# Kernel optimization log

Hardware: AMD Instinct MI355X
Metric: run time of the kernel (lower is better)

## Reference

```python
import jax, jax.numpy as jnp
import numpy as np

B, S, T = 256, 512, 20
VOCAB, E, H, SKIP = 100000, 25, 128, 64


def _lstm_scan(x, skip, mask, K, R, Sk, b):
    # x:[S,B,E], skip:[S,B,SKIP], mask:[S,B] bool. Keras RNN mask semantics:
    # masked steps carry previous h/c and emit previous h.
    Bn = x.shape[1]
    Hn = R.shape[0]
    def step(carry, inp):
        h, c = carry
        xt, st, mt = inp
        z = xt @ K + h @ R + st @ Sk + b            # [B,4H]
        zi, zf, zg, zo = jnp.split(z, 4, axis=-1)
        cn = jax.nn.sigmoid(zf) * c + jax.nn.sigmoid(zi) * jnp.tanh(zg)
        hn = jax.nn.sigmoid(zo) * jnp.tanh(cn)
        m = mt[:, None]
        h2 = jnp.where(m, hn, h)
        c2 = jnp.where(m, cn, c)
        return (h2, c2), h2
    init = (jnp.zeros((Bn, Hn), x.dtype), jnp.zeros((Bn, Hn), x.dtype))
    (hF, cF), hs = jax.lax.scan(step, init, (x, skip, mask))
    return hs, hF


def setup_inputs() -> dict:
    key = jax.random.key(0)
    ks = jax.random.split(key, 20)
    p = lambda k, shp: jax.random.normal(k, shp, dtype=jnp.float32) * 0.05
    inp = {
        "input_tags": jax.random.randint(ks[0], (B, S, T), 0, VOCAB, dtype=jnp.int32),
        "embedded_skips": jax.random.normal(ks[1], (B, S, SKIP), dtype=jnp.float32),
        "emb_table": p(ks[2], (VOCAB, E)),
        "kernel_f": p(ks[3], (E, 4 * H)),
        "rec_f": p(ks[4], (H, 4 * H)),
        "skip_f": p(ks[5], (SKIP, 4 * H)),
        "bias_f": jnp.zeros((4 * H,), jnp.float32),
        "kernel_b": p(ks[6], (E, 4 * H)),
        "rec_b": p(ks[7], (H, 4 * H)),
        "skip_b": p(ks[8], (SKIP, 4 * H)),
        "bias_b": jnp.zeros((4 * H,), jnp.float32),
        "Wk": p(ks[9], (2 * H, H)),
        "bk": jnp.zeros((H,), jnp.float32),
        "Wq": p(ks[10], (H, H)),
        "bq": jnp.zeros((H,), jnp.float32),
        "We": p(ks[11], (H, 1)),
        "be": jnp.zeros((1,), jnp.float32),
    }
    return inp


def reference(input_tags, embedded_skips, emb_table,
              kernel_f, rec_f, skip_f, bias_f,
              kernel_b, rec_b, skip_b, bias_b,
              Wk, bk, Wq, bq, We, be):
    mask3 = input_tags != 0                          # [B,S,T]
    emb = emb_table[input_tags]                      # [B,S,T,E]
    num_mask = mask3.astype(emb.dtype)
    summed = jnp.sum(emb * num_mask[..., None], axis=2)   # [B,S,E]
    denom = jnp.sum(num_mask, axis=2)                     # [B,S]
    denom = jnp.where(denom == 0, jnp.ones_like(denom), denom)
    gru_inp = summed / denom[..., None]                   # [B,S,E]
    step_mask = mask3[:, :, 0]                            # [B,S]

    # time-major for scan
    x_t = jnp.swapaxes(gru_inp, 0, 1)
    s_t = jnp.swapaxes(embedded_skips, 0, 1)
    m_t = jnp.swapaxes(step_mask, 0, 1)

    hs_f, h_fwd = _lstm_scan(x_t, s_t, m_t, kernel_f, rec_f, skip_f, bias_f)
    hs_b_rev, _ = _lstm_scan(x_t[::-1], s_t[::-1], m_t[::-1], kernel_b, rec_b, skip_b, bias_b)
    hs_b = hs_b_rev[::-1]
    out = jnp.swapaxes(jnp.concatenate([hs_f, hs_b], axis=-1), 0, 1)  # [B,S,2H]

    keys = out @ Wk + bk                                  # [B,S,H]
    queries = (h_fwd @ Wq + bq)[:, None, :]               # [B,1,H]
    energy = jnp.tanh(keys + queries) @ We + be           # [B,S,1]
    energy = energy + (1.0 - step_mask.astype(energy.dtype))[..., None] * -1e9
    weights = jax.nn.softmax(energy, axis=1)
    context = jnp.sum(weights * out, axis=1)              # [B,2H]
    return context
```

## Files before the change

### kernel.cpp

```cpp
#include <hip/hip_runtime.h>
#include <math.h>

#define Bb 256
#define Ss 512
#define Tt 20
#define Ee 25
#define Hh 128
#define SKIPn 64
#define H4n 512
#define BSn (Bb*Ss)
#define MG 4
#define HP 160
#define LOG2E 1.4426950408889634f

typedef _Float16 f16x8 __attribute__((ext_vector_type(8)));
typedef float f32x4 __attribute__((ext_vector_type(4)));

__device__ __forceinline__ float rcpf(float x) { return __builtin_amdgcn_rcpf(x); }
__device__ __forceinline__ float exp2f_(float x) { return __builtin_amdgcn_exp2f(x); }

__device__ __forceinline__ void lgkm_barrier() {
    __asm__ __volatile__("" ::: "memory");
    __builtin_amdgcn_s_waitcnt(0xC07F);
    __builtin_amdgcn_s_barrier();
    __asm__ __volatile__("" ::: "memory");
}

__global__ void pool_kernel(const int* __restrict__ tags,
                            const float* __restrict__ table,
                            _Float16* __restrict__ gru16, float* __restrict__ maskf,
                            float* __restrict__ maskt) {
    int group = blockIdx.x * 8 + (threadIdx.x >> 5);
    int lane = threadIdx.x & 31;
    if (group >= BSn) return;
    int b = group >> 9;
    int t = group & (Ss - 1);
    const int* tg = tags + (size_t)group * Tt;
    const int el = (lane < Ee) ? lane : (Ee - 1);

    int tagv[Tt];
#pragma unroll
    for (int tt = 0; tt < Tt; tt++) tagv[tt] = tg[tt];

    float vv[Tt];
#pragma unroll
    for (int tt = 0; tt < Tt; tt++)
        vv[tt] = table[(size_t)tagv[tt] * Ee + el];

    float acc = 0.0f;
    int cnt = 0;
#pragma unroll
    for (int tt = 0; tt < Tt; tt++) {
        const bool nz = (tagv[tt] != 0);
        cnt += nz ? 1 : 0;
        acc += nz ? vv[tt] : 0.0f;
    }
    float scale = rcpf((float)(cnt > 0 ? cnt : 1));
    float v = (lane < Ee) ? acc * scale : 0.0f;
    gru16[((size_t)t * Bb + b) * 32 + lane] = (_Float16)v;
    if (lane == 0) {
        float m = (tagv[0] != 0) ? 1.0f : 0.0f;
        maskf[group] = m;
        maskt[(size_t)t * Bb + b] = m;
    }
}

__global__ void __launch_bounds__(256)
cvt_kernel(const float* __restrict__ in, _Float16* __restrict__ out) {
    size_t i = ((size_t)blockIdx.x * 256 + threadIdx.x) * 8;
    f32x4 a = *(const f32x4*)(in + i);
    f32x4 b = *(const f32x4*)(in + i + 4);
    f16x8 o;
#pragma unroll
    for (int j = 0; j < 4; j++) { o[j] = (_Float16)a[j]; o[j + 4] = (_Float16)b[j]; }
    *(f16x8*)(out + i) = o;
}

__global__ void __launch_bounds__(512)
__attribute__((amdgpu_waves_per_eu(2, 2)))
scan_kernel(const _Float16* __restrict__ gru16, const _Float16* __restrict__ skips16,
            const float* __restrict__ maskt,
            const float* __restrict__ Kf, const float* __restrict__ Rf,
            const float* __restrict__ Skf, const float* __restrict__ bf,
            const float* __restrict__ Kb, const float* __restrict__ Rb,
            const float* __restrict__ Skb, const float* __restrict__ bb,
            _Float16* __restrict__ hs16, float* __restrict__ hfwd)
{
    __shared__ __align__(16) _Float16 h16[2 * MG * HP];

    const int tid = threadIdx.x;
    const int lane = tid & 63;
    const int w = tid >> 6;
    const int l16 = lane & 15;
    const int q = lane >> 4;
    const int mb = l16 >> 2;
    const int bg = blockIdx.x & 63;
    const int dir = blockIdx.x >> 6;
    const int b0 = bg * MG;
    const int col = 16 * w + l16;

    const float* Kw = dir ? Kb : Kf;
    const float* Rw = dir ? Rb : Rf;
    const float* Sw = dir ? Skb : Skf;
    const float* bw = dir ? bb : bf;

    const float gs[4] = {LOG2E, LOG2E, 2.0f * LOG2E, LOG2E};

    f16x8 bfr[7][4];
#pragma unroll
    for (int kt = 0; kt < 7; kt++) {
#pragma unroll
        for (int g = 0; g < 4; g++) {
            const int n = g * Hh + col;
            f16x8 v;
#pragma unroll
            for (int j = 0; j < 8; j++) {
                const int k = 32 * kt + 8 * q + j;
                float x;
                if (k < 32)        x = (k < Ee) ? Kw[k * H4n + n] : 0.0f;
                else if (k < 160)  x = Rw[(k - 32) * H4n + n];
                else               x = Sw[(k - 160) * H4n + n];
                v[j] = (_Float16)(x * gs[g]);
            }
            bfr[kt][g] = v;
        }
    }
    float biasv[4];
#pragma unroll
    for (int g = 0; g < 4; g++) biasv[g] = bw[g * Hh + col] * gs[g];

    for (int idx = tid; idx < 2 * MG * HP; idx += 512) h16[idx] = (_Float16)0.0f;

    const _Float16* srow = skips16 + (size_t)(b0 + mb) * Ss * SKIPn;
    float c = 0.0f, h = 0.0f;

    _Float16* hsp = hs16 + ((size_t)(b0 + q) * Ss + (dir ? Ss - 1 : 0)) * (2 * Hh)
                    + dir * Hh + col;
    const ptrdiff_t odelta = dir ? -(2 * Hh) : (2 * Hh);

    auto issue_xs = [&](f16x8& xf, f16x8& s0, f16x8& s1, int i) {
        const int ii = (i < Ss) ? i : (Ss - 1);
        const int t = dir ? (Ss - 1 - ii) : ii;
        xf = *(const f16x8*)(gru16 + ((size_t)t * Bb + b0 + mb) * 32 + 8 * q);
        const _Float16* sp = srow + (size_t)t * SKIPn;
        s0 = *(const f16x8*)(sp + 8 * q);
        s1 = *(const f16x8*)(sp + 32 + 8 * q);
    };
    auto issue_m = [&](float& mk, int i) {
        const int ii = (i < Ss) ? i : (Ss - 1);
        const int t = dir ? (Ss - 1 - ii) : ii;
        mk = maskt[(size_t)t * Bb + b0 + q];
    };

    f16x8 xA, xB, sA0, sA1, sB0, sB1;
    float mA, mB;
    issue_xs(xA, sA0, sA1, 0); issue_m(mA, 0);
    issue_xs(xB, sB0, sB1, 1); issue_m(mB, 1);
    __syncthreads();

    auto body = [&](int i, f16x8& xf, f16x8& s0, f16x8& s1, float& mkv) {
        const _Float16* hb = h16 + (i & 1) * (MG * HP);
        const f16x8 ah0 = *(const f16x8*)(hb + mb * HP +  0 + 8 * q);
        const f16x8 ah1 = *(const f16x8*)(hb + mb * HP + 32 + 8 * q);
        const f16x8 ah2 = *(const f16x8*)(hb + mb * HP + 64 + 8 * q);
        const f16x8 ah3 = *(const f16x8*)(hb + mb * HP + 96 + 8 * q);

        f32x4 acc[4];
#pragma unroll
        for (int g = 0; g < 4; g++) {
            f32x4 a = {biasv[g], biasv[g], biasv[g], biasv[g]};
            acc[g] = a;
        }
#pragma unroll
        for (int g = 0; g < 4; g++) {
            acc[g] = __builtin_amdgcn_mfma_f32_16x16x32_f16(xf, bfr[0][g], acc[g], 0, 0, 0);
            acc[g] = __builtin_amdgcn_mfma_f32_16x16x32_f16(s0, bfr[5][g], acc[g], 0, 0, 0);
            acc[g] = __builtin_amdgcn_mfma_f32_16x16x32_f16(s1, bfr[6][g], acc[g], 0, 0, 0);
        }
        issue_xs(xf, s0, s1, i + 2);
#pragma unroll
        for (int g = 0; g < 4; g++) {
            acc[g] = __builtin_amdgcn_mfma_f32_16x16x32_f16(ah0, bfr[1][g], acc[g], 0, 0, 0);
            acc[g] = __builtin_amdgcn_mfma_f32_16x16x32_f16(ah1, bfr[2][g], acc[g], 0, 0, 0);
            acc[g] = __builtin_amdgcn_mfma_f32_16x16x32_f16(ah2, bfr[3][g], acc[g], 0, 0, 0);
            acc[g] = __builtin_amdgcn_mfma_f32_16x16x32_f16(ah3, bfr[4][g], acc[g], 0, 0, 0);
        }

        const float mk = mkv;
        issue_m(mkv, i + 2);
        const float zi = acc[0][0], zf = acc[1][0], zg = acc[2][0], zo = acc[3][0];
        const float ei = exp2f_(fminf(-zi, 88.0f));
        const float ef = exp2f_(fminf(-zf, 88.0f));
        const float eg = exp2f_(fminf(-zg, 88.0f));
        const float eo = exp2f_(fminf(-zo, 88.0f));
        const float pi = 1.0f + ei, pg = 1.0f + eg, pf = 1.0f + ef;
        const float p  = pi * pg;
        const float t1 = (1.0f - eg) * pf;
        const float cn = fmaf(c, p, t1) * rcpf(pf * p);
        const float ec = exp2f_(fminf(cn * (-2.0f * LOG2E), 88.0f));
        const float hn = (1.0f - ec) * rcpf((1.0f + eo) * (1.0f + ec));
        const bool mm = (mk != 0.0f);
        c = mm ? cn : c;
        h = mm ? hn : h;

        _Float16* hw = h16 + ((i + 1) & 1) * (MG * HP);
        hw[q * HP + col] = (_Float16)h;
        *hsp = (_Float16)h;
        hsp += odelta;
        lgkm_barrier();
    };

#pragma unroll 1
    for (int i = 0; i < Ss; i += 2) {
        body(i,     xA, sA0, sA1, mA);
        body(i + 1, xB, sB0, sB1, mB);
    }

    if (dir == 0) hfwd[(size_t)(b0 + q) * Hh + col] = h;
}

__global__ void __launch_bounds__(512)
attn_kernel(const _Float16* __restrict__ hs16, const float* __restrict__ hfwd,
            const float* __restrict__ Wq, const float* __restrict__ bq,
            const float* __restrict__ bk,
            const float* __restrict__ Wk, const float* __restrict__ We,
            const float* __restrict__ maskf, float* __restrict__ outp)
{
    __shared__ float hfl[Hh];
    __shared__ float qpart[4][Hh];
    __shared__ float qtot_s[Hh];
    __shared__ float epart[8][Ss];
    __shared__ float ws2[Ss];
    __shared__ float redm[8], reds[8];
    __shared__ float ctxp[16][2 * Hh + 1];

    const int tid = threadIdx.x;
    const int lane = tid & 63;
    const int w = tid >> 6;
    const int l16 = lane & 15;
    const int q = lane >> 4;
    const int b = blockIdx.x;
    const int j = 16 * w + l16;

    f16x8 bk16[8];
#pragma unroll
    for (int kt = 0; kt < 8; kt++) {
        f16x8 v;
#pragma unroll
        for (int jj = 0; jj < 8; jj++)
            v[jj] = (_Float16)Wk[(32 * kt + 8 * q + jj) * Hh + j];
        bk16[kt] = v;
    }
    const float wej = We[j];

    if (tid < Hh) hfl[tid] = hfwd[(size_t)b * Hh + tid];
    __syncthreads();
    {
        const int jj = tid & 127, seg = tid >> 7;
        float p = 0.0f;
#pragma unroll
        for (int k = 0; k < 32; k++)
            p += hfl[32 * seg + k] * Wq[(32 * seg + k) * Hh + jj];
        qpart[seg][jj] = p;
    }
    __syncthreads();
    if (tid < Hh)
        qtot_s[tid] = qpart[0][tid] + qpart[1][tid] + qpart[2][tid] + qpart[3][tid]
                      + bq[tid] + bk[tid];
    __syncthreads();
    const float qj = qtot_s[j];

    const _Float16* hb = hs16 + (size_t)b * Ss * (2 * Hh);
#pragma unroll 1
    for (int st = 0; st < 32; st++) {
        const int s0 = st * 16;
        const _Float16* arow = hb + (size_t)(s0 + l16) * (2 * Hh) + 8 * q;
        f32x4 acc = {0.f, 0.f, 0.f, 0.f};
#pragma unroll
        for (int kt = 0; kt < 8; kt++) {
            const f16x8 a = *(const f16x8*)(arow + 32 * kt);
            acc = __builtin_amdgcn_mfma_f32_16x16x32_f16(a, bk16[kt], acc, 0, 0, 0);
        }
        float vals[4];
#pragma unroll
        for (int r = 0; r < 4; r++) {
            const float x = acc[r] + qj;
            const float e = exp2f_(fminf(x * (-2.0f * LOG2E), 80.0f));
            vals[r] = (1.0f - e) * rcpf(1.0f + e) * wej;
        }
#pragma unroll
        for (int m = 1; m < 16; m <<= 1) {
#pragma unroll
            for (int r = 0; r < 4; r++) vals[r] += __shfl_xor(vals[r], m);
        }
        if (l16 == 0) {
#pragma unroll
            for (int r = 0; r < 4; r++) epart[w][s0 + 4 * q + r] = vals[r];
        }
    }
    __syncthreads();

    {
        float e = 0.0f;
#pragma unroll
        for (int ww = 0; ww < 8; ww++) e += epart[ww][tid];
        e += (1.0f - maskf[(size_t)b * Ss + tid]) * -1e9f;
        float mx = e;
#pragma unroll
        for (int off = 32; off > 0; off >>= 1) mx = fmaxf(mx, __shfl_xor(mx, off));
        if (lane == 0) redm[w] = mx;
        __syncthreads();
        mx = redm[0];
#pragma unroll
        for (int ww = 1; ww < 8; ww++) mx = fmaxf(mx, redm[ww]);
        const float p = exp2f_((e - mx) * LOG2E);
        float sm = p;
#pragma unroll
        for (int off = 32; off > 0; off >>= 1) sm += __shfl_xor(sm, off);
        if (lane == 0) reds[w] = sm;
        __syncthreads();
        sm = reds[0] + reds[1] + reds[2] + reds[3] + reds[4] + reds[5] + reds[6] + reds[7];
        ws2[(tid & 31) * 16 + (tid >> 5)] = p * rcpf(sm);
    }
    __syncthreads();

    {
        const int cg = tid >> 4;
        const int seg = tid & 15;
        float a[8];
#pragma unroll
        for (int jj = 0; jj < 8; jj++) a[jj] = 0.0f;
#pragma unroll 4
        for (int sg = 0; sg < 32; sg++) {
            const int s = seg * 32 + sg;
            const float wv = ws2[sg * 16 + seg];
            const f16x8 hv = *(const f16x8*)(hb + (size_t)s * (2 * Hh) + 8 * cg);
#pragma unroll
            for (int jj = 0; jj < 8; jj++) a[jj] = fmaf(wv, (float)hv[jj], a[jj]);
        }
#pragma unroll
        for (int jj = 0; jj < 8; jj++) ctxp[seg][8 * cg + jj] = a[jj];
    }
    __syncthreads();
    if (tid < 2 * Hh) {
        float s = 0.0f;
#pragma unroll
        for (int seg = 0; seg < 16; seg++) s += ctxp[seg][tid];
        outp[(size_t)b * (2 * Hh) + tid] = s;
    }
}

extern "C" void kernel_launch(void* const* d_in, const int* in_sizes, int n_in,
                              void* d_out, int out_size, void* d_ws, size_t ws_size,
                              hipStream_t stream) {
    const int*   tags  = (const int*)d_in[0];
    const float* skips = (const float*)d_in[1];
    const float* table = (const float*)d_in[2];
    const float* Kf    = (const float*)d_in[3];
    const float* Rf    = (const float*)d_in[4];
    const float* Skf   = (const float*)d_in[5];
    const float* bf    = (const float*)d_in[6];
    const float* Kb    = (const float*)d_in[7];
    const float* Rb    = (const float*)d_in[8];
    const float* Skb   = (const float*)d_in[9];
    const float* bb    = (const float*)d_in[10];
    const float* Wk    = (const float*)d_in[11];
    const float* bk    = (const float*)d_in[12];
    const float* Wq    = (const float*)d_in[13];
    const float* bq    = (const float*)d_in[14];
    const float* We    = (const float*)d_in[15];

    char* ws = (char*)d_ws;
    _Float16* gru16   = (_Float16*)ws; ws += (size_t)BSn * 32 * 2;
    _Float16* skips16 = (_Float16*)ws; ws += (size_t)BSn * SKIPn * 2;
    float* maskf  = (float*)ws;  ws += (size_t)BSn * 4;
    float* maskt  = (float*)ws;  ws += (size_t)BSn * 4;
    _Float16* hs16 = (_Float16*)ws; ws += (size_t)BSn * 2 * Hh * 2;
    float* hfwd   = (float*)ws;  ws += (size_t)Bb * Hh * 4;

    pool_kernel<<<BSn / 8, 256, 0, stream>>>(tags, table, gru16, maskf, maskt);
    cvt_kernel<<<BSn * SKIPn / (256 * 8), 256, 0, stream>>>(skips, skips16);
    scan_kernel<<<128, 512, 0, stream>>>(gru16, skips16, maskt,
                                         Kf, Rf, Skf, bf,
                                         Kb, Rb, Skb, bb,
                                         hs16, hfwd);
    attn_kernel<<<Bb, 512, 0, stream>>>(hs16, hfwd, Wq, bq, bk, Wk, We, maskf,
                                        (float*)d_out);
}
```

Baseline: 551.3 us.

## Precompute input/skip gate projections in a parallel GEMM before the LSTM scan

Splits the LSTM into a fully parallel MFMA kernel that computes x@K + skip@Sk + bias for all timesteps into an fp16 z buffer. A lighter scan kernel then only does the recurrent h@R matmul per step and loads the precomputed gates with a prefetch two steps ahead. This takes the input and skip projections off the serial critical path of the 512-step recurrence. The cost is a large fp16 intermediate buffer, extra memory traffic and fp16 rounding of the gate preactivations. There are fallbacks for a chunked variant with carry state and for the original fused scan, chosen by workspace size.

```diff
diff --git a/kernel.cpp b/kernel.cpp
--- a/kernel.cpp
+++ b/kernel.cpp
@@ -11,9 +11,11 @@
 #define BSn (Bb*Ss)
 #define MG 4
 #define HP 160
+#define ZROWS 256
 #define LOG2E 1.4426950408889634f
 
 typedef _Float16 f16x8 __attribute__((ext_vector_type(8)));
+typedef _Float16 f16x4 __attribute__((ext_vector_type(4)));
 typedef float f32x4 __attribute__((ext_vector_type(4)));
 
 __device__ __forceinline__ float rcpf(float x) { return __builtin_amdgcn_rcpf(x); }
@@ -65,26 +67,249 @@
     }
 }
 
+template<bool TR>
 __global__ void __launch_bounds__(256)
 cvt_kernel(const float* __restrict__ in, _Float16* __restrict__ out) {
-    size_t i = ((size_t)blockIdx.x * 256 + threadIdx.x) * 8;
-    f32x4 a = *(const f32x4*)(in + i);
-    f32x4 b = *(const f32x4*)(in + i + 4);
-    f16x8 o;
-#pragma unroll
-    for (int j = 0; j < 4; j++) { o[j] = (_Float16)a[j]; o[j + 4] = (_Float16)b[j]; }
-    *(f16x8*)(out + i) = o;
-}
-
+    size_t id = (size_t)blockIdx.x * 256 + threadIdx.x;
+    if (TR) {
+        size_t bt = id >> 3;
+        const int c8 = (int)(id & 7);
+        const int b = (int)(bt >> 9);
+        const int t = (int)(bt & (Ss - 1));
+        const float* ip = in + bt * SKIPn + c8 * 8;
+        f32x4 a = *(const f32x4*)(ip);
+        f32x4 bv = *(const f32x4*)(ip + 4);
+        f16x8 o;
+#pragma unroll
+        for (int j = 0; j < 4; j++) { o[j] = (_Float16)a[j]; o[j + 4] = (_Float16)bv[j]; }
+        *(f16x8*)(out + ((size_t)t * Bb + b) * SKIPn + c8 * 8) = o;
+    } else {
+        size_t i = id * 8;
+        f32x4 a = *(const f32x4*)(in + i);
+        f32x4 bv = *(const f32x4*)(in + i + 4);
+        f16x8 o;
+#pragma unroll
+        for (int j = 0; j < 4; j++) { o[j] = (_Float16)a[j]; o[j + 4] = (_Float16)bv[j]; }
+        *(f16x8*)(out + i) = o;
+    }
+}
+
+template<int CH>
+__global__ void __launch_bounds__(512)
+zxs_kernel(const _Float16* __restrict__ gru16, const _Float16* __restrict__ sk16,
+           const float* __restrict__ Kf, const float* __restrict__ Skf, const float* __restrict__ bf,
+           const float* __restrict__ Kb, const float* __restrict__ Skb, const float* __restrict__ bb,
+           _Float16* __restrict__ zbuf, int k)
+{
+    const int tid = threadIdx.x;
+    const int lane = tid & 63;
+    const int w = tid >> 6;
+    const int l16 = lane & 15;
+    const int q = lane >> 4;
+    const int dir = blockIdx.x & 1;
+    const int rg = blockIdx.x >> 1;
+    const size_t lrow0 = (size_t)rg * ZROWS;
+    const size_t grow0 = ((size_t)(dir ? (Ss - CH * (k + 1)) : (CH * k)) * Bb) + lrow0;
+    const int col = 16 * w + l16;
+
+    const float* Kw = dir ? Kb : Kf;
+    const float* Sw = dir ? Skb : Skf;
+    const float* bw = dir ? bb : bf;
+    const float gs[4] = {LOG2E, LOG2E, 2.0f * LOG2E, LOG2E};
+
+    f16x8 bx[4], bs0[4], bs1[4];
+#pragma unroll
+    for (int g = 0; g < 4; g++) {
+        const int n = g * Hh + col;
+        f16x8 vx, v0, v1;
+#pragma unroll
+        for (int j = 0; j < 8; j++) {
+            const int kk = 8 * q + j;
+            vx[j] = (_Float16)(((kk < Ee) ? Kw[kk * H4n + n] : 0.0f) * gs[g]);
+            v0[j] = (_Float16)(Sw[kk * H4n + n] * gs[g]);
+            v1[j] = (_Float16)(Sw[(32 + kk) * H4n + n] * gs[g]);
+        }
+        bx[g] = vx; bs0[g] = v0; bs1[g] = v1;
+    }
+    float biasv[4];
+#pragma unroll
+    for (int g = 0; g < 4; g++) biasv[g] = bw[g * Hh + col] * gs[g];
+
+    auto lda = [&](f16x8& ax, f16x8& a0, f16x8& a1, int ch) {
+        const size_t r = grow0 + 16 * ch + l16;
+        ax = *(const f16x8*)(gru16 + r * 32 + 8 * q);
+        a0 = *(const f16x8*)(sk16 + r * SKIPn + 8 * q);
+        a1 = *(const f16x8*)(sk16 + r * SKIPn + 32 + 8 * q);
+    };
+
+    f16x8 ax, a0, a1, nx, n0, n1;
+    lda(ax, a0, a1, 0);
+#pragma unroll 1
+    for (int ch = 0; ch < ZROWS / 16; ch++) {
+        const int chn = (ch + 1 < ZROWS / 16) ? ch + 1 : ch;
+        lda(nx, n0, n1, chn);
+        f32x4 acc[4];
+#pragma unroll
+        for (int g = 0; g < 4; g++) {
+            f32x4 a = {biasv[g], biasv[g], biasv[g], biasv[g]};
+            acc[g] = a;
+        }
+#pragma unroll
+        for (int g = 0; g < 4; g++)
+            acc[g] = __builtin_amdgcn_mfma_f32_16x16x32_f16(ax, bx[g], acc[g], 0, 0, 0);
+#pragma unroll
+        for (int g = 0; g < 4; g++)
+            acc[g] = __builtin_amdgcn_mfma_f32_16x16x32_f16(a0, bs0[g], acc[g], 0, 0, 0);
+#pragma unroll
+        for (int g = 0; g < 4; g++)
+            acc[g] = __builtin_amdgcn_mfma_f32_16x16x32_f16(a1, bs1[g], acc[g], 0, 0, 0);
+
+        _Float16* op = zbuf + (((size_t)dir * CH * Bb + lrow0 + 16 * ch + 4 * q) * 128 + col) * 4;
+#pragma unroll
+        for (int r = 0; r < 4; r++) {
+            f16x4 o;
+#pragma unroll
+            for (int g = 0; g < 4; g++) o[g] = (_Float16)acc[g][r];
+            *(f16x4*)(op + (size_t)r * 512) = o;
+        }
+        ax = nx; a0 = n0; a1 = n1;
+    }
+}
+
+template<int CH>
 __global__ void __launch_bounds__(512)
 __attribute__((amdgpu_waves_per_eu(2, 2)))
-scan_kernel(const _Float16* __restrict__ gru16, const _Float16* __restrict__ skips16,
-            const float* __restrict__ maskt,
-            const float* __restrict__ Kf, const float* __restrict__ Rf,
-            const float* __restrict__ Skf, const float* __restrict__ bf,
-            const float* __restrict__ Kb, const float* __restrict__ Rb,
-            const float* __restrict__ Skb, const float* __restrict__ bb,
-            _Float16* __restrict__ hs16, float* __restrict__ hfwd)
+scan_split(const _Float16* __restrict__ zbuf, const float* __restrict__ maskt,
+           const float* __restrict__ Rf, const float* __restrict__ Rb,
+           _Float16* __restrict__ hs16, float* __restrict__ hfwd,
+           float2* __restrict__ carry, int k)
+{
+    constexpr int NCH = Ss / CH;
+    __shared__ __align__(16) _Float16 h16[2 * MG * HP];
+
+    const int tid = threadIdx.x;
+    const int lane = tid & 63;
+    const int w = tid >> 6;
+    const int l16 = lane & 15;
+    const int q = lane >> 4;
+    const int mb = l16 >> 2;
+    const int bg = blockIdx.x & 63;
+    const int dir = blockIdx.x >> 6;
+    const int b0 = bg * MG;
+    const int col = 16 * w + l16;
+
+    const float* Rw = dir ? Rb : Rf;
+    const float gs[4] = {LOG2E, LOG2E, 2.0f * LOG2E, LOG2E};
+
+    f16x8 hfr[4][4];
+#pragma unroll
+    for (int kt = 0; kt < 4; kt++) {
+#pragma unroll
+        for (int g = 0; g < 4; g++) {
+            const int n = g * Hh + col;
+            f16x8 v;
+#pragma unroll
+            for (int j = 0; j < 8; j++)
+                v[j] = (_Float16)(Rw[(32 * kt + 8 * q + j) * H4n + n] * gs[g]);
+            hfr[kt][g] = v;
+        }
+    }
+
+    const int cid = (dir * Bb + b0 + q) * Hh + col;
+    float c = 0.0f, h = 0.0f;
+    if (k > 0) { float2 hc = carry[cid]; h = hc.x; c = hc.y; }
+
+    h16[q * HP + col] = (_Float16)h;
+
+    const _Float16* zbase = zbuf + ((size_t)dir * CH * Bb + (size_t)(b0 + q)) * 512 + col * 4;
+
+    const int t0 = dir ? (Ss - 1 - CH * k) : (CH * k);
+    _Float16* hsp = hs16 + ((size_t)(b0 + q) * Ss + t0) * (2 * Hh) + dir * Hh + col;
+    const ptrdiff_t odelta = dir ? -(2 * Hh) : (2 * Hh);
+
+    auto issue_z = [&](f16x4& z, int i) {
+        const int ii = (i < CH) ? i : (CH - 1);
+        const int tl = dir ? (CH - 1 - ii) : ii;
+        z = *(const f16x4*)(zbase + (size_t)tl * (Bb * 512));
+    };
+    auto issue_m = [&](float& mk, int i) {
+        const int ii = (i < CH) ? i : (CH - 1);
+        const int tg = dir ? (Ss - 1 - CH * k - ii) : (CH * k + ii);
+        mk = maskt[(size_t)tg * Bb + b0 + q];
+    };
+
+    f16x4 zA, zB;
+    float mA, mB;
+    issue_z(zA, 0); issue_m(mA, 0);
+    issue_z(zB, 1); issue_m(mB, 1);
+    __syncthreads();
+
+    auto body = [&](int i, f16x4& zf4, float& mkv) {
+        const _Float16* hb = h16 + (i & 1) * (MG * HP);
+        const f16x8 ah0 = *(const f16x8*)(hb + mb * HP +  0 + 8 * q);
+        const f16x8 ah1 = *(const f16x8*)(hb + mb * HP + 32 + 8 * q);
+        const f16x8 ah2 = *(const f16x8*)(hb + mb * HP + 64 + 8 * q);
+        const f16x8 ah3 = *(const f16x8*)(hb + mb * HP + 96 + 8 * q);
+
+        f32x4 acc[4];
+#pragma unroll
+        for (int g = 0; g < 4; g++) {
+            const float zv = (float)zf4[g];
+            f32x4 a = {zv, zv, zv, zv};
+            acc[g] = a;
+        }
+        issue_z(zf4, i + 2);
+#pragma unroll
+        for (int g = 0; g < 4; g++) {
+            acc[g] = __builtin_amdgcn_mfma_f32_16x16x32_f16(ah0, hfr[0][g], acc[g], 0, 0, 0);
+            acc[g] = __builtin_amdgcn_mfma_f32_16x16x32_f16(ah1, hfr[1][g], acc[g], 0, 0, 0);
+            acc[g] = __builtin_amdgcn_mfma_f32_16x16x32_f16(ah2, hfr[2][g], acc[g], 0, 0, 0);
+            acc[g] = __builtin_amdgcn_mfma_f32_16x16x32_f16(ah3, hfr[3][g], acc[g], 0, 0, 0);
+        }
+
+        const float mk = mkv;
+        issue_m(mkv, i + 2);
+        const float zi = acc[0][0], zf = acc[1][0], zg = acc[2][0], zo = acc[3][0];
+        const float ei = exp2f_(fminf(-zi, 88.0f));
+        const float ef = exp2f_(fminf(-zf, 88.0f));
+        const float eg = exp2f_(fminf(-zg, 88.0f));
+        const float eo = exp2f_(fminf(-zo, 88.0f));
+        const float pi = 1.0f + ei, pg = 1.0f + eg, pf = 1.0f + ef;
+        const float p  = pi * pg;
+        const float t1 = (1.0f - eg) * pf;
+        const float cn = fmaf(c, p, t1) * rcpf(pf * p);
+        const float ec = exp2f_(fminf(cn * (-2.0f * LOG2E), 88.0f));
+        const float hn = (1.0f - ec) * rcpf((1.0f + eo) * (1.0f + ec));
+        const bool mm = (mk != 0.0f);
+        c = mm ? cn : c;
+        h = mm ? hn : h;
+
+        _Float16* hw = h16 + ((i + 1) & 1) * (MG * HP);
+        hw[q * HP + col] = (_Float16)h;
+        *hsp = (_Float16)h;
+        hsp += odelta;
+        lgkm_barrier();
+    };
+
+#pragma unroll 1
+    for (int i = 0; i < CH; i += 2) {
+        body(i,     zA, mA);
+        body(i + 1, zB, mB);
+    }
+
+    if (k + 1 < NCH) carry[cid] = make_float2(h, c);
+    if (dir == 0 && k + 1 == NCH) hfwd[(size_t)(b0 + q) * Hh + col] = h;
+}
+
+__global__ void __launch_bounds__(512)
+__attribute__((amdgpu_waves_per_eu(2, 2)))
+scan_fused(const _Float16* __restrict__ gru16, const _Float16* __restrict__ skips16,
+           const float* __restrict__ maskt,
+           const float* __restrict__ Kf, const float* __restrict__ Rf,
+           const float* __restrict__ Skf, const float* __restrict__ bf,
+           const float* __restrict__ Kb, const float* __restrict__ Rb,
+           const float* __restrict__ Skb, const float* __restrict__ bb,
+           _Float16* __restrict__ hs16, float* __restrict__ hfwd)
 {
     __shared__ __align__(16) _Float16 h16[2 * MG * HP];
 
@@ -370,20 +595,73 @@
     const float* bq    = (const float*)d_in[14];
     const float* We    = (const float*)d_in[15];
 
+    const size_t SZ_GRU = (size_t)BSn * 32 * 2;
+    const size_t SZ_SKT = (size_t)BSn * SKIPn * 2;
+    const size_t SZ_HS  = (size_t)BSn * 2 * Hh * 2;
+    const size_t SZ_MSK = (size_t)BSn * 4;
+    const size_t SZ_HF  = (size_t)Bb * Hh * 4;
+    const size_t SZ_CAR = (size_t)2 * Bb * Hh * 8;
+    const size_t SZ_ZF  = (size_t)2 * Ss * Bb * 512 * 2;
+    const size_t SZ_ZC  = (size_t)2 * 128 * Bb * 512 * 2;
+
+    const size_t NEED_FULL  = SZ_ZF + SZ_HS + 2 * SZ_MSK + SZ_HF;
+    const size_t NEED_CHUNK = SZ_ZC + SZ_GRU + SZ_SKT + SZ_HS + 2 * SZ_MSK + SZ_HF + SZ_CAR;
+
     char* ws = (char*)d_ws;
-    _Float16* gru16   = (_Float16*)ws; ws += (size_t)BSn * 32 * 2;
-    _Float16* skips16 = (_Float16*)ws; ws += (size_t)BSn * SKIPn * 2;
-    float* maskf  = (float*)ws;  ws += (size_t)BSn * 4;
-    float* maskt  = (float*)ws;  ws += (size_t)BSn * 4;
-    _Float16* hs16 = (_Float16*)ws; ws += (size_t)BSn * 2 * Hh * 2;
-    float* hfwd   = (float*)ws;  ws += (size_t)Bb * Hh * 4;
-
-    pool_kernel<<<BSn / 8, 256, 0, stream>>>(tags, table, gru16, maskf, maskt);
-    cvt_kernel<<<BSn * SKIPn / (256 * 8), 256, 0, stream>>>(skips, skips16);
-    scan_kernel<<<128, 512, 0, stream>>>(gru16, skips16, maskt,
-                                         Kf, Rf, Skf, bf,
-                                         Kb, Rb, Skb, bb,
-                                         hs16, hfwd);
-    attn_kernel<<<Bb, 512, 0, stream>>>(hs16, hfwd, Wq, bq, bk, Wk, We, maskf,
-                                        (float*)d_out);
-}
+
+    if (ws_size >= NEED_FULL) {
+        _Float16* zbuf  = (_Float16*)ws; ws += SZ_ZF;
+        _Float16* hs16  = (_Float16*)ws;
+        _Float16* gru16 = (_Float16*)ws;
+        _Float16* sk16t = (_Float16*)(ws + SZ_GRU);
+        ws += SZ_HS;
+        float* maskf = (float*)ws; ws += SZ_MSK;
+        float* maskt = (float*)ws; ws += SZ_MSK;
+        float* hfwd  = (float*)ws; ws += SZ_HF;
+
+        pool_kernel<<<BSn / 8, 256, 0, stream>>>(tags, table, gru16, maskf, maskt);
+        cvt_kernel<true><<<BSn * SKIPn / (256 * 8), 256, 0, stream>>>(skips, sk16t);
+        zxs_kernel<Ss><<<2 * (Ss * Bb / ZROWS), 512, 0, stream>>>(
+            gru16, sk16t, Kf, Skf, bf, Kb, Skb, bb, zbuf, 0);
+        scan_split<Ss><<<128, 512, 0, stream>>>(zbuf, maskt, Rf, Rb, hs16, hfwd,
+                                                (float2*)hfwd , 0);
+        attn_kernel<<<Bb, 512, 0, stream>>>(hs16, hfwd, Wq, bq, bk, Wk, We, maskf,
+                                            (float*)d_out);
+    } else if (ws_size >= NEED_CHUNK) {
+        _Float16* zbuf  = (_Float16*)ws; ws += SZ_ZC;
+        _Float16* gru16 = (_Float16*)ws; ws += SZ_GRU;
+        _Float16* sk16t = (_Float16*)ws; ws += SZ_SKT;
+        _Float16* hs16  = (_Float16*)ws; ws += SZ_HS;
+        float* maskf = (float*)ws; ws += SZ_MSK;
+        float* maskt = (float*)ws; ws += SZ_MSK;
+        float* hfwd  = (float*)ws; ws += SZ_HF;
+        float2* carry = (float2*)ws; ws += SZ_CAR;
+
+        pool_kernel<<<BSn / 8, 256, 0, stream>>>(tags, table, gru16, maskf, maskt);
+        cvt_kernel<true><<<BSn * SKIPn / (256 * 8), 256, 0, stream>>>(skips, sk16t);
+        for (int k = 0; k < 4; k++) {
+            zxs_kernel<128><<<2 * (128 * Bb / ZROWS), 512, 0, stream>>>(
+                gru16, sk16t, Kf, Skf, bf, Kb, Skb, bb, zbuf, k);
+            scan_split<128><<<128, 512, 0, stream>>>(zbuf, maskt, Rf, Rb, hs16, hfwd,
+                                                     carry, k);
+        }
+        attn_kernel<<<Bb, 512, 0, stream>>>(hs16, hfwd, Wq, bq, bk, Wk, We, maskf,
+                                            (float*)d_out);
+    } else {
+        _Float16* gru16   = (_Float16*)ws; ws += SZ_GRU;
+        _Float16* skips16 = (_Float16*)ws; ws += SZ_SKT;
+        float* maskf = (float*)ws; ws += SZ_MSK;
+        float* maskt = (float*)ws; ws += SZ_MSK;
+        _Float16* hs16 = (_Float16*)ws; ws += SZ_HS;
+        float* hfwd  = (float*)ws; ws += SZ_HF;
+
+        pool_kernel<<<BSn / 8, 256, 0, stream>>>(tags, table, gru16, maskf, maskt);
+        cvt_kernel<false><<<BSn * SKIPn / (256 * 8), 256, 0, stream>>>(skips, skips16);
+        scan_fused<<<128, 512, 0, stream>>>(gru16, skips16, maskt,
+                                            Kf, Rf, Skf, bf,
+                                            Kb, Rb, Skb, bb,
+                                            hs16, hfwd);
+        attn_kernel<<<Bb, 512, 0, stream>>>(hs16, hfwd, Wq, bq, bk, Wk, We, maskf,
+                                            (float*)d_out);
+    }
+}
```

After: 599.9 us. 8.8% more time.

## Precompute input projections per 16-step chunk in LDS; stage attention tiles through LDS

Applied to the files above, without the earlier changes.

The scan kernel stops doing the x and skip input-projection MFMAs inside every serial step. Instead it computes them in batches of 16 timesteps into an LDS buffer in fp16, so each recurrent step only runs the four hidden-state MFMAs per gate plus one LDS read. This shortens the serial critical path and lowers register pressure, at the cost of fp16 rounding of the pre-activations and an extra barrier per chunk. The attention kernel double-buffers its hs tiles through LDS with a prefetch of the next tile, and the context-reduction thread mapping is changed. The mask buffer gets padding so that prefetches past the end stay in bounds.

```diff
diff --git a/kernel.cpp b/kernel.cpp
--- a/kernel.cpp
+++ b/kernel.cpp
@@ -11,9 +11,12 @@
 #define BSn (Bb*Ss)
 #define MG 4
 #define HP 160
+#define ZP 520
+#define AP 264
 #define LOG2E 1.4426950408889634f
 
 typedef _Float16 f16x8 __attribute__((ext_vector_type(8)));
+typedef _Float16 f16x4 __attribute__((ext_vector_type(4)));
 typedef float f32x4 __attribute__((ext_vector_type(4)));
 
 __device__ __forceinline__ float rcpf(float x) { return __builtin_amdgcn_rcpf(x); }
@@ -78,7 +81,7 @@
 
 __global__ void __launch_bounds__(512)
 __attribute__((amdgpu_waves_per_eu(2, 2)))
-scan_kernel(const _Float16* __restrict__ gru16, const _Float16* __restrict__ skips16,
+scan_kernel(const _Float16* __restrict__ gru16, const _Float16* __restrict__ sk16,
             const float* __restrict__ maskt,
             const float* __restrict__ Kf, const float* __restrict__ Rf,
             const float* __restrict__ Skf, const float* __restrict__ bf,
@@ -87,6 +90,7 @@
             _Float16* __restrict__ hs16, float* __restrict__ hfwd)
 {
     __shared__ __align__(16) _Float16 h16[2 * MG * HP];
+    __shared__ __align__(16) _Float16 zlds[64 * ZP];
 
     const int tid = threadIdx.x;
     const int lane = tid & 63;
@@ -103,92 +107,90 @@
     const float* Rw = dir ? Rb : Rf;
     const float* Sw = dir ? Skb : Skf;
     const float* bw = dir ? bb : bf;
-
     const float gs[4] = {LOG2E, LOG2E, 2.0f * LOG2E, LOG2E};
 
-    f16x8 bfr[7][4];
-#pragma unroll
-    for (int kt = 0; kt < 7; kt++) {
+    f16x8 hfr[4][4];
+#pragma unroll
+    for (int kt = 0; kt < 4; kt++) {
 #pragma unroll
         for (int g = 0; g < 4; g++) {
             const int n = g * Hh + col;
             f16x8 v;
 #pragma unroll
-            for (int j = 0; j < 8; j++) {
-                const int k = 32 * kt + 8 * q + j;
-                float x;
-                if (k < 32)        x = (k < Ee) ? Kw[k * H4n + n] : 0.0f;
-                else if (k < 160)  x = Rw[(k - 32) * H4n + n];
-                else               x = Sw[(k - 160) * H4n + n];
-                v[j] = (_Float16)(x * gs[g]);
-            }
-            bfr[kt][g] = v;
-        }
-    }
-    float biasv[4];
-#pragma unroll
-    for (int g = 0; g < 4; g++) biasv[g] = bw[g * Hh + col] * gs[g];
+            for (int j = 0; j < 8; j++)
+                v[j] = (_Float16)(Rw[(32 * kt + 8 * q + j) * H4n + n] * gs[g]);
+            hfr[kt][g] = v;
+        }
+    }
+    f16x8 bx[4], bs0[4], bs1[4];
+    f32x4 biasA[4];
+#pragma unroll
+    for (int g = 0; g < 4; g++) {
+        const int n = g * Hh + col;
+        f16x8 vx, v0, v1;
+#pragma unroll
+        for (int j = 0; j < 8; j++) {
+            const int kk = 8 * q + j;
+            vx[j] = (_Float16)(((kk < Ee) ? Kw[kk * H4n + n] : 0.0f) * gs[g]);
+            v0[j] = (_Float16)(Sw[kk * H4n + n] * gs[g]);
+            v1[j] = (_Float16)(Sw[(32 + kk) * H4n + n] * gs[g]);
+        }
+        bx[g] = vx; bs0[g] = v0; bs1[g] = v1;
+        const float bv = bw[g * Hh + col] * gs[g];
+        f32x4 ba = {bv, bv, bv, bv};
+        biasA[g] = ba;
+    }
+    const f32x4 zacc4 = {0.0f, 0.0f, 0.0f, 0.0f};
 
     for (int idx = tid; idx < 2 * MG * HP; idx += 512) h16[idx] = (_Float16)0.0f;
 
-    const _Float16* srow = skips16 + (size_t)(b0 + mb) * Ss * SKIPn;
     float c = 0.0f, h = 0.0f;
+
+    const int tsub = l16 >> 2, bbn = l16 & 3;
+    const int tg0 = dir ? (Ss - 1 - tsub) : tsub;
+    const _Float16* px = gru16 + ((size_t)tg0 * Bb + b0 + bbn) * 32 + 8 * q;
+    const _Float16* ps = sk16 + ((size_t)(b0 + bbn) * Ss + tg0) * SKIPn + 8 * q;
+    const ptrdiff_t pxd = (dir ? -4 : 4) * (ptrdiff_t)(Bb * 32);
+    const ptrdiff_t psd = (dir ? -4 : 4) * (ptrdiff_t)SKIPn;
+
+    const float* mptr = maskt + (size_t)(dir ? (Ss - 1) : 0) * Bb + b0 + q;
+    const ptrdiff_t mdelta = dir ? -(ptrdiff_t)Bb : (ptrdiff_t)Bb;
+    float mA = mptr[0], mB = mptr[mdelta];
+    const float* mpf = mptr + 2 * mdelta;
 
     _Float16* hsp = hs16 + ((size_t)(b0 + q) * Ss + (dir ? Ss - 1 : 0)) * (2 * Hh)
                     + dir * Hh + col;
     const ptrdiff_t odelta = dir ? -(2 * Hh) : (2 * Hh);
 
-    auto issue_xs = [&](f16x8& xf, f16x8& s0, f16x8& s1, int i) {
-        const int ii = (i < Ss) ? i : (Ss - 1);
-        const int t = dir ? (Ss - 1 - ii) : ii;
-        xf = *(const f16x8*)(gru16 + ((size_t)t * Bb + b0 + mb) * 32 + 8 * q);
-        const _Float16* sp = srow + (size_t)t * SKIPn;
-        s0 = *(const f16x8*)(sp + 8 * q);
-        s1 = *(const f16x8*)(sp + 32 + 8 * q);
-    };
-    auto issue_m = [&](float& mk, int i) {
-        const int ii = (i < Ss) ? i : (Ss - 1);
-        const int t = dir ? (Ss - 1 - ii) : ii;
-        mk = maskt[(size_t)t * Bb + b0 + q];
-    };
-
-    f16x8 xA, xB, sA0, sA1, sB0, sB1;
-    float mA, mB;
-    issue_xs(xA, sA0, sA1, 0); issue_m(mA, 0);
-    issue_xs(xB, sB0, sB1, 1); issue_m(mB, 1);
-    __syncthreads();
-
-    auto body = [&](int i, f16x8& xf, f16x8& s0, f16x8& s1, float& mkv) {
+    f16x8 nax = *(const f16x8*)px;
+    f16x8 na0 = *(const f16x8*)ps;
+    f16x8 na1 = *(const f16x8*)(ps + 32);
+
+    __syncthreads();
+
+    auto body = [&](int i, float& mkv) {
         const _Float16* hb = h16 + (i & 1) * (MG * HP);
         const f16x8 ah0 = *(const f16x8*)(hb + mb * HP +  0 + 8 * q);
         const f16x8 ah1 = *(const f16x8*)(hb + mb * HP + 32 + 8 * q);
         const f16x8 ah2 = *(const f16x8*)(hb + mb * HP + 64 + 8 * q);
         const f16x8 ah3 = *(const f16x8*)(hb + mb * HP + 96 + 8 * q);
+        const f16x4 z4 = *(const f16x4*)(zlds + ((i & 15) * 4 + q) * ZP + col * 4);
 
         f32x4 acc[4];
 #pragma unroll
         for (int g = 0; g < 4; g++) {
-            f32x4 a = {biasv[g], biasv[g], biasv[g], biasv[g]};
-            acc[g] = a;
-        }
-#pragma unroll
-        for (int g = 0; g < 4; g++) {
-            acc[g] = __builtin_amdgcn_mfma_f32_16x16x32_f16(xf, bfr[0][g], acc[g], 0, 0, 0);
-            acc[g] = __builtin_amdgcn_mfma_f32_16x16x32_f16(s0, bfr[5][g], acc[g], 0, 0, 0);
-            acc[g] = __builtin_amdgcn_mfma_f32_16x16x32_f16(s1, bfr[6][g], acc[g], 0, 0, 0);
-        }
-        issue_xs(xf, s0, s1, i + 2);
-#pragma unroll
-        for (int g = 0; g < 4; g++) {
-            acc[g] = __builtin_amdgcn_mfma_f32_16x16x32_f16(ah0, bfr[1][g], acc[g], 0, 0, 0);
-            acc[g] = __builtin_amdgcn_mfma_f32_16x16x32_f16(ah1, bfr[2][g], acc[g], 0, 0, 0);
-            acc[g] = __builtin_amdgcn_mfma_f32_16x16x32_f16(ah2, bfr[3][g], acc[g], 0, 0, 0);
-            acc[g] = __builtin_amdgcn_mfma_f32_16x16x32_f16(ah3, bfr[4][g], acc[g], 0, 0, 0);
+            acc[g] = __builtin_amdgcn_mfma_f32_16x16x32_f16(ah0, hfr[0][g], zacc4, 0, 0, 0);
+            acc[g] = __builtin_amdgcn_mfma_f32_16x16x32_f16(ah1, hfr[1][g], acc[g], 0, 0, 0);
+            acc[g] = __builtin_amdgcn_mfma_f32_16x16x32_f16(ah2, hfr[2][g], acc[g], 0, 0, 0);
+            acc[g] = __builtin_amdgcn_mfma_f32_16x16x32_f16(ah3, hfr[3][g], acc[g], 0, 0, 0);
         }
 
         const float mk = mkv;
-        issue_m(mkv, i + 2);
-        const float zi = acc[0][0], zf = acc[1][0], zg = acc[2][0], zo = acc[3][0];
+        mkv = *mpf; mpf += mdelta;
+        const float zi = acc[0][0] + (float)z4[0];
+        const float zf = acc[1][0] + (float)z4[1];
+        const float zg = acc[2][0] + (float)z4[2];
+        const float zo = acc[3][0] + (float)z4[3];
         const float ei = exp2f_(fminf(-zi, 88.0f));
         const float ef = exp2f_(fminf(-zf, 88.0f));
         const float eg = exp2f_(fminf(-zg, 88.0f));
@@ -210,10 +212,41 @@
         lgkm_barrier();
     };
 
+    int i = 0;
 #pragma unroll 1
-    for (int i = 0; i < Ss; i += 2) {
-        body(i,     xA, sA0, sA1, mA);
-        body(i + 1, xB, sB0, sB1, mB);
+    for (int k = 0; k < 32; ++k) {
+#pragma unroll
+        for (int tile = 0; tile < 4; ++tile) {
+            const f16x8 ax = nax, a0 = na0, a1 = na1;
+            px += pxd; ps += psd;
+            if ((k < 31) | (tile < 3)) {
+                nax = *(const f16x8*)px;
+                na0 = *(const f16x8*)ps;
+                na1 = *(const f16x8*)(ps + 32);
+            }
+            f32x4 zc[4];
+#pragma unroll
+            for (int g = 0; g < 4; g++) {
+                zc[g] = __builtin_amdgcn_mfma_f32_16x16x32_f16(ax, bx[g],  biasA[g], 0, 0, 0);
+                zc[g] = __builtin_amdgcn_mfma_f32_16x16x32_f16(a0, bs0[g], zc[g], 0, 0, 0);
+                zc[g] = __builtin_amdgcn_mfma_f32_16x16x32_f16(a1, bs1[g], zc[g], 0, 0, 0);
+            }
+            _Float16* zw = zlds + ((tile * 4 + q) * 4) * ZP + col * 4;
+#pragma unroll
+            for (int r = 0; r < 4; r++) {
+                f16x4 o;
+                o[0] = (_Float16)zc[0][r]; o[1] = (_Float16)zc[1][r];
+                o[2] = (_Float16)zc[2][r]; o[3] = (_Float16)zc[3][r];
+                *(f16x4*)(zw + r * ZP) = o;
+            }
+        }
+        lgkm_barrier();
+#pragma unroll 1
+        for (int j = 0; j < 16; j += 2) {
+            body(i,     mA);
+            body(i + 1, mB);
+            i += 2;
+        }
     }
 
     if (dir == 0) hfwd[(size_t)(b0 + q) * Hh + col] = h;
@@ -233,6 +266,7 @@
     __shared__ float ws2[Ss];
     __shared__ float redm[8], reds[8];
     __shared__ float ctxp[16][2 * Hh + 1];
+    __shared__ __align__(16) _Float16 atile[2][16 * AP];
 
     const int tid = threadIdx.x;
     const int lane = tid & 63;
@@ -271,14 +305,22 @@
     const float qj = qtot_s[j];
 
     const _Float16* hb = hs16 + (size_t)b * Ss * (2 * Hh);
+    const int srow = tid >> 5;
+    const int spart = tid & 31;
+    *(f16x8*)(&atile[0][srow * AP + spart * 8]) =
+        *(const f16x8*)(hb + (size_t)srow * (2 * Hh) + spart * 8);
+    __syncthreads();
 #pragma unroll 1
     for (int st = 0; st < 32; st++) {
+        const int p = st & 1;
+        f16x8 sreg;
+        if (st < 31)
+            sreg = *(const f16x8*)(hb + (size_t)((st + 1) * 16 + srow) * (2 * Hh) + spart * 8);
         const int s0 = st * 16;
-        const _Float16* arow = hb + (size_t)(s0 + l16) * (2 * Hh) + 8 * q;
         f32x4 acc = {0.f, 0.f, 0.f, 0.f};
 #pragma unroll
         for (int kt = 0; kt < 8; kt++) {
-            const f16x8 a = *(const f16x8*)(arow + 32 * kt);
+            const f16x8 a = *(const f16x8*)(&atile[p][l16 * AP + kt * 32 + 8 * q]);
             acc = __builtin_amdgcn_mfma_f32_16x16x32_f16(a, bk16[kt], acc, 0, 0, 0);
         }
         float vals[4];
@@ -297,8 +339,10 @@
 #pragma unroll
             for (int r = 0; r < 4; r++) epart[w][s0 + 4 * q + r] = vals[r];
         }
-    }
-    __syncthreads();
+        if (st < 31)
+            *(f16x8*)(&atile[p ^ 1][srow * AP + spart * 8]) = sreg;
+        __syncthreads();
+    }
 
     {
         float e = 0.0f;
@@ -325,8 +369,8 @@
     __syncthreads();
 
     {
-        const int cg = tid >> 4;
-        const int seg = tid & 15;
+        const int cg = tid & 31;
+        const int seg = tid >> 5;
         float a[8];
 #pragma unroll
         for (int jj = 0; jj < 8; jj++) a[jj] = 0.0f;
@@ -371,16 +415,17 @@
     const float* We    = (const float*)d_in[15];
 
     char* ws = (char*)d_ws;
-    _Float16* gru16   = (_Float16*)ws; ws += (size_t)BSn * 32 * 2;
-    _Float16* skips16 = (_Float16*)ws; ws += (size_t)BSn * SKIPn * 2;
-    float* maskf  = (float*)ws;  ws += (size_t)BSn * 4;
-    float* maskt  = (float*)ws;  ws += (size_t)BSn * 4;
+    _Float16* gru16 = (_Float16*)ws; ws += (size_t)BSn * 32 * 2;
+    _Float16* sk16  = (_Float16*)ws; ws += (size_t)BSn * SKIPn * 2;
+    float* maskf = (float*)ws; ws += (size_t)BSn * 4;
+    float* maskt_base = (float*)ws; ws += ((size_t)BSn + 4 * Bb) * 4;
+    float* maskt = maskt_base + 2 * Bb;
     _Float16* hs16 = (_Float16*)ws; ws += (size_t)BSn * 2 * Hh * 2;
-    float* hfwd   = (float*)ws;  ws += (size_t)Bb * Hh * 4;
+    float* hfwd  = (float*)ws; ws += (size_t)Bb * Hh * 4;
 
     pool_kernel<<<BSn / 8, 256, 0, stream>>>(tags, table, gru16, maskf, maskt);
-    cvt_kernel<<<BSn * SKIPn / (256 * 8), 256, 0, stream>>>(skips, skips16);
-    scan_kernel<<<128, 512, 0, stream>>>(gru16, skips16, maskt,
+    cvt_kernel<<<BSn * SKIPn / (256 * 8), 256, 0, stream>>>(skips, sk16);
+    scan_kernel<<<128, 512, 0, stream>>>(gru16, sk16, maskt,
                                          Kf, Rf, Skf, bf,
                                          Kb, Rb, Skb, bb,
                                          hs16, hfwd);
```

Result: faster. 539.7 us (-2.1%).
